# Optimization experiments

Measured on AMD Instinct MI355X. Metric: run time of the kernel, lower is better.

Reference implementation:

```python
import jax, jax.numpy as jnp
import numpy as np

B, H, W, C = 64, 56, 56, 192
HEADS = 6
WIN = (7, 7)
SHIFT = (3, 3)
N = WIN[0] * WIN[1]  # tokens per window = 49
EPS = 1e-5


def _rel_pos_index(ws):
    # standard Swin relative position index, shape (N, N), values in [0, (2wh-1)(2ww-1))
    coords = np.stack(np.meshgrid(np.arange(ws[0]), np.arange(ws[1]), indexing='ij'))
    cf = coords.reshape(2, -1)
    rel = (cf[:, :, None] - cf[:, None, :]).transpose(1, 2, 0)  # N,N,2
    rel[..., 0] += ws[0] - 1
    rel[..., 1] += ws[1] - 1
    rel[..., 0] *= 2 * ws[1] - 1
    return rel.sum(-1)


def _swin_attn_mask(h, w, ws, ss):
    # cyclic-shift attention mask, shape (nW, N, N), values {0, -100}
    img = np.zeros((h, w), dtype=np.float32)
    cnt = 0
    for hs in (slice(0, -ws[0]), slice(-ws[0], -ss[0]), slice(-ss[0], None)):
        for wsl in (slice(0, -ws[1]), slice(-ws[1], -ss[1]), slice(-ss[1], None)):
            img[hs, wsl] = cnt
            cnt += 1
    m = img.reshape(h // ws[0], ws[0], w // ws[1], ws[1]).transpose(0, 2, 1, 3).reshape(-1, N)
    am = m[:, None, :] - m[:, :, None]
    return np.where(am != 0, -100.0, 0.0).astype(np.float32)


def setup_inputs() -> dict:
    key = jax.random.key(0)
    ks = jax.random.split(key, 5)
    x = jax.random.normal(ks[0], (B, H, W, C), dtype=jnp.float32)
    mask_matrix = jnp.asarray(_swin_attn_mask(H, W, WIN, SHIFT))
    gamma = jnp.ones((C,), jnp.float32)
    beta = jnp.zeros((C,), jnp.float32)
    w_qkv = jax.random.normal(ks[1], (C, 3 * C), jnp.float32) * 0.02
    b_qkv = jnp.zeros((3 * C,), jnp.float32)
    rel_table = jax.random.normal(ks[2], ((2 * WIN[0] - 1) * (2 * WIN[1] - 1), HEADS), jnp.float32) * 0.02
    w_proj = jax.random.normal(ks[3], (C, C), jnp.float32) * 0.02
    b_proj = jnp.zeros((C,), jnp.float32)
    return {"x": x, "gamma": gamma, "beta": beta, "w_qkv": w_qkv, "b_qkv": b_qkv,
            "rel_table": rel_table, "w_proj": w_proj, "b_proj": b_proj,
            "mask_matrix": mask_matrix}


def reference(x, gamma, beta, w_qkv, b_qkv, rel_table, w_proj, b_proj, mask_matrix):
    b, h, w, c = x.shape
    hd = c // HEADS
    scale = hd ** -0.5

    # norm1 (LayerNorm over channels)
    mu = jnp.mean(x, axis=-1, keepdims=True)
    var = jnp.var(x, axis=-1, keepdims=True)
    x = (x - mu) * jax.lax.rsqrt(var + EPS) * gamma + beta

    # cyclic shift (H,W divisible by window -> no padding)
    sx = jnp.roll(x, shift=(-SHIFT[0], -SHIFT[1]), axis=(1, 2))

    # window partition -> (B*nW, N, C)
    nh, nw = h // WIN[0], w // WIN[1]
    win = sx.reshape(b, nh, WIN[0], nw, WIN[1], c).transpose(0, 1, 3, 2, 4, 5)
    win = win.reshape(-1, N, c)

    # window attention with relative position bias + shift mask
    qkv = (win @ w_qkv + b_qkv).reshape(-1, N, 3, HEADS, hd).transpose(2, 0, 3, 1, 4)
    q, k, v = qkv[0], qkv[1], qkv[2]  # (B_, heads, N, hd)
    attn = jnp.einsum('bhnd,bhmd->bhnm', q * scale, k)
    rpi = _rel_pos_index(WIN)
    bias = rel_table[rpi.reshape(-1)].reshape(N, N, HEADS).transpose(2, 0, 1)  # heads,N,N
    attn = attn + bias[None]
    nW = mask_matrix.shape[0]
    attn = attn.reshape(b, nW, HEADS, N, N) + mask_matrix[None, :, None]
    attn = jax.nn.softmax(attn.reshape(-1, HEADS, N, N), axis=-1)
    out = jnp.einsum('bhnm,bhmd->bhnd', attn, v).transpose(0, 2, 1, 3).reshape(-1, N, c)
    out = out @ w_proj + b_proj

    # window reverse -> (B,H,W,C)
    out = out.reshape(b, nh, nw, WIN[0], WIN[1], c).transpose(0, 1, 3, 2, 4, 5).reshape(b, h, w, c)

    # reverse cyclic shift
    return jnp.roll(out, shift=(SHIFT[0], SHIFT[1]), axis=(1, 2))
```

## Files before the change

kernel.cpp:

```cpp
#include <hip/hip_runtime.h>
#include <hip/hip_bf16.h>
#include <math.h>

typedef __bf16 bf16;
typedef __bf16 bf16x4 __attribute__((ext_vector_type(4)));
typedef __bf16 bf16x8 __attribute__((ext_vector_type(8)));
typedef float f32x4 __attribute__((ext_vector_type(4)));
typedef unsigned int u32x4 __attribute__((ext_vector_type(4)));

#define NHEADS 6
#define CDIM 192
#define IMG 56
#define NTOK 49
#define SHIFTV 3
#define XSTR 200
#define VSTR 72
#define LOG2E 1.4426950408889634f
#define SCALE 0.17677669529663687f
#define MSKNEG (-100.0f * LOG2E)

#define MFMA(a, b, c) __builtin_amdgcn_mfma_f32_16x16x32_bf16(a, b, c, 0, 0, 0)

static __device__ __forceinline__ unsigned pack2bf(float lo, float hi) {
    unsigned short a = __builtin_bit_cast(unsigned short, (bf16)lo);
    unsigned short b = __builtin_bit_cast(unsigned short, (bf16)hi);
    return (unsigned)a | ((unsigned)b << 16);
}

__global__ void prep_weights(const float* __restrict__ w_qkv, const float* __restrict__ w_proj,
                             bf16* __restrict__ wqkvT, bf16* __restrict__ wprojT) {
    int i = blockIdx.x * 256 + threadIdx.x;
    if (i < 576 * 192) {
        int n = i / 192, k = i % 192;
        wqkvT[i] = (bf16)w_qkv[k * 576 + n];
    }
    if (i < 192 * 192) {
        int n = i / 192, k = i % 192;
        wprojT[i] = (bf16)w_proj[k * 192 + n];
    }
}

__global__ __launch_bounds__(512, 4) void swin_block(
    const float* __restrict__ x, const float* __restrict__ gamma, const float* __restrict__ beta,
    const bf16* __restrict__ wqkvT, const float* __restrict__ b_qkv,
    const float* __restrict__ rel_table, const bf16* __restrict__ wprojT,
    const float* __restrict__ b_proj, float* __restrict__ out)
{
    __shared__ __align__(16) bf16 BufA[64 * XSTR];
    __shared__ __align__(16) bf16 BufB[64 * XSTR];
    __shared__ __align__(16) bf16 VTs[CDIM * VSTR];
    __shared__ bf16 biasS[169 * NHEADS];

    const int blk  = blockIdx.x;
    const int bimg = blk >> 6;
    const int wy   = (blk >> 3) & 7;
    const int wx   = blk & 7;
    const int tid  = threadIdx.x;
    const int wave = tid >> 6;
    const int lane = tid & 63;
    const int lr   = lane & 15;
    const int lq   = lane >> 4;
    const int h0   = wave & 1;
    const int cg   = wave >> 1;

    for (int i = tid; i < 169 * NHEADS; i += 512) biasS[i] = (bf16)(rel_table[i] * LOG2E);

    {
        const int c0 = lr * 12;
        const f32x4 gm0 = *(const f32x4*)&gamma[c0], gm1 = *(const f32x4*)&gamma[c0 + 4], gm2 = *(const f32x4*)&gamma[c0 + 8];
        const f32x4 bt0 = *(const f32x4*)&beta[c0],  bt1 = *(const f32x4*)&beta[c0 + 4],  bt2 = *(const f32x4*)&beta[c0 + 8];
        #pragma unroll
        for (int it = 0; it < 2; ++it) {
            const int t = it * 32 + wave * 4 + lq;
            if (t < NTOK) {
                int ty = t / 7, tx = t % 7;
                int oy = wy * 7 + ty + SHIFTV; if (oy >= IMG) oy -= IMG;
                int ox = wx * 7 + tx + SHIFTV; if (ox >= IMG) ox -= IMG;
                const float* xp = x + (((size_t)bimg * IMG + oy) * IMG + ox) * CDIM + c0;
                f32x4 v0 = *(const f32x4*)(xp), v1 = *(const f32x4*)(xp + 4), v2 = *(const f32x4*)(xp + 8);
                float s = 0.f, ss = 0.f;
                #pragma unroll
                for (int r = 0; r < 4; ++r) {
                    s  += v0[r] + v1[r] + v2[r];
                    ss += v0[r] * v0[r] + v1[r] * v1[r] + v2[r] * v2[r];
                }
                #pragma unroll
                for (int off = 1; off < 16; off <<= 1) { s += __shfl_xor(s, off); ss += __shfl_xor(ss, off); }
                float mu  = s * (1.f / 192.f);
                float var = ss * (1.f / 192.f) - mu * mu;
                float rs  = rsqrtf(var + 1e-5f);
                bf16x4 o0, o1, o2;
                #pragma unroll
                for (int r = 0; r < 4; ++r) {
                    o0[r] = (bf16)((v0[r] - mu) * rs * gm0[r] + bt0[r]);
                    o1[r] = (bf16)((v1[r] - mu) * rs * gm1[r] + bt1[r]);
                    o2[r] = (bf16)((v2[r] - mu) * rs * gm2[r] + bt2[r]);
                }
                *(bf16x4*)&BufA[t * XSTR + c0    ] = o0;
                *(bf16x4*)&BufA[t * XSTR + c0 + 4] = o1;
                *(bf16x4*)&BufA[t * XSTR + c0 + 8] = o2;
            } else {
                bf16x4 z = {(bf16)0.f, (bf16)0.f, (bf16)0.f, (bf16)0.f};
                *(bf16x4*)&BufA[t * XSTR + c0    ] = z;
                *(bf16x4*)&BufA[t * XSTR + c0 + 4] = z;
                *(bf16x4*)&BufA[t * XSTR + c0 + 8] = z;
            }
        }
    }
    __syncthreads();

    {
        bf16x8 afrag[2][6];
        #pragma unroll
        for (int mm = 0; mm < 2; ++mm)
            #pragma unroll
            for (int k = 0; k < 6; ++k)
                afrag[mm][k] = *(const bf16x8*)&BufA[(32 * h0 + 16 * mm + lr) * XSTR + k * 32 + lq * 8];
        __syncthreads();

        const bf16* wbase = wqkvT + (size_t)lr * CDIM + lq * 8;
#define WPTR(nt) (wbase + (size_t)(nt) * (16 * CDIM))
#define LOADW6(dst, p) do { const bf16* _p = (p); \
    _Pragma("unroll") for (int k = 0; k < 6; ++k) dst[k] = *(const bf16x8*)(_p + k * 32); } while (0)
#define COMP_QK(buf, nt, dstb) do { \
    f32x4 a0 = {0.f,0.f,0.f,0.f}, a1 = {0.f,0.f,0.f,0.f}; \
    _Pragma("unroll") for (int k = 0; k < 6; ++k) { \
        a0 = MFMA(buf[k], afrag[0][k], a0); \
        a1 = MFMA(buf[k], afrag[1][k], a1); } \
    const int ccl_ = ((nt) % 12) * 16 + 4 * lq; \
    const f32x4 bq_ = *(const f32x4*)&b_qkv[(nt) * 16 + 4 * lq]; \
    bf16x4 v0_, v1_; \
    _Pragma("unroll") for (int r = 0; r < 4; ++r) { v0_[r] = (bf16)(a0[r] + bq_[r]); v1_[r] = (bf16)(a1[r] + bq_[r]); } \
    *(bf16x4*)&dstb[(32 * h0 + lr) * XSTR + ccl_] = v0_; \
    *(bf16x4*)&dstb[(32 * h0 + 16 + lr) * XSTR + ccl_] = v1_; } while (0)
#define COMP_V(buf, nt) do { \
    f32x4 a0 = {0.f,0.f,0.f,0.f}, a1 = {0.f,0.f,0.f,0.f}; \
    _Pragma("unroll") for (int k = 0; k < 6; ++k) { \
        a0 = MFMA(afrag[0][k], buf[k], a0); \
        a1 = MFMA(afrag[1][k], buf[k], a1); } \
    const int cc_ = ((nt) - 24) * 16 + lr; \
    const float bb_ = b_qkv[384 + cc_]; \
    bf16x4 v0_, v1_; \
    _Pragma("unroll") for (int r = 0; r < 4; ++r) { v0_[r] = (bf16)(a0[r] + bb_); v1_[r] = (bf16)(a1[r] + bb_); } \
    *(bf16x4*)&VTs[cc_ * VSTR + 32 * h0 + 4 * lq] = v0_; \
    *(bf16x4*)&VTs[cc_ * VSTR + 32 * h0 + 16 + 4 * lq] = v1_; } while (0)

        bf16x8 bA[6], bB[6];
        LOADW6(bA, WPTR(cg));
        LOADW6(bB, WPTR(cg + 4));  COMP_QK(bA, cg,      BufB);
        LOADW6(bA, WPTR(cg + 8));  COMP_QK(bB, cg + 4,  BufB);
        LOADW6(bB, WPTR(cg + 12)); COMP_QK(bA, cg + 8,  BufB);
        LOADW6(bA, WPTR(cg + 16)); COMP_QK(bB, cg + 12, BufA);
        LOADW6(bB, WPTR(cg + 20)); COMP_QK(bA, cg + 16, BufA);
        LOADW6(bA, WPTR(cg + 24)); COMP_QK(bB, cg + 20, BufA);
        LOADW6(bB, WPTR(cg + 28)); COMP_V (bA, cg + 24);
        LOADW6(bA, WPTR(cg + 32)); COMP_V (bB, cg + 28);
                                   COMP_V (bA, cg + 32);
    }
    __syncthreads();

    {
        const int m  = wave & 3;
        const int hg = wave >> 2;
        const int i  = 16 * m + lr;
        const int ic = i < NTOK ? i : NTOK - 1;
        const int iy = ic / 7, ix = ic % 7;
        const int ay = wy * 7 + iy, ax = wx * 7 + ix;
        const int ryi = (ay < 49) ? 0 : ((ay < 53) ? 1 : 2);
        const int rxi = (ax < 49) ? 0 : ((ax < 53) ? 1 : 2);
        int   rp[4][4];
        float msk[4][4];
        #pragma unroll
        for (int n = 0; n < 4; ++n)
            #pragma unroll
            for (int r = 0; r < 4; ++r) {
                int j = 16 * n + 4 * lq + r;
                if (j < NTOK) {
                    int jy = j / 7, jx = j % 7;
                    rp[n][r] = ((iy - jy + 6) * 13 + (ix - jx + 6)) * NHEADS;
                    int by = wy * 7 + jy, bx = wx * 7 + jx;
                    int ryj = (by < 49) ? 0 : ((by < 53) ? 1 : 2);
                    int rxj = (bx < 49) ? 0 : ((bx < 53) ? 1 : 2);
                    msk[n][r] = (ryi == ryj && rxi == rxj) ? 0.f : MSKNEG;
                } else { rp[n][r] = 0; msk[n][r] = -1e30f; }
            }
        const int src0 = lr + 32 * (lq & 1);
        const float SC = SCALE * LOG2E;

        #pragma unroll
        for (int hh = 0; hh < 3; ++hh) {
            const int h = hg * 3 + hh;
            bf16x8 bq = *(const bf16x8*)&BufB[(16 * m + lr) * XSTR + h * 32 + lq * 8];
            f32x4 st[4];
            #pragma unroll
            for (int n = 0; n < 4; ++n) {
                bf16x8 ak = *(const bf16x8*)&BufA[(16 * n + lr) * XSTR + h * 32 + lq * 8];
                st[n] = MFMA(ak, bq, (f32x4{0.f, 0.f, 0.f, 0.f}));
            }
            float umax = -1e30f;
            #pragma unroll
            for (int n = 0; n < 4; ++n)
                #pragma unroll
                for (int r = 0; r < 4; ++r) {
                    st[n][r] = fmaf(st[n][r], SC, msk[n][r]) + (float)biasS[rp[n][r] + h];
                    umax = fmaxf(umax, st[n][r]);
                }
            umax = fmaxf(umax, __shfl_xor(umax, 16));
            umax = fmaxf(umax, __shfl_xor(umax, 32));
            float sum = 0.f;
            #pragma unroll
            for (int n = 0; n < 4; ++n)
                #pragma unroll
                for (int r = 0; r < 4; ++r) {
                    float e = exp2f(st[n][r] - umax);
                    st[n][r] = e; sum += e;
                }
            sum += __shfl_xor(sum, 16);
            sum += __shfl_xor(sum, 32);
            const float inv = 1.f / sum;
            unsigned pk[4][2];
            #pragma unroll
            for (int n = 0; n < 4; ++n)
                #pragma unroll
                for (int s = 0; s < 2; ++s)
                    pk[n][s] = pack2bf(st[n][2 * s] * inv, st[n][2 * s + 1] * inv);
            u32x4 ptw0, ptw1;
            #pragma unroll
            for (int w = 0; w < 4; ++w) {
                int srcl = src0 + 16 * (w >> 1);
                int s = w & 1;
                unsigned a0 = (unsigned)__shfl((int)pk[0][s], srcl);
                unsigned b0 = (unsigned)__shfl((int)pk[1][s], srcl);
                unsigned a1 = (unsigned)__shfl((int)pk[2][s], srcl);
                unsigned b1 = (unsigned)__shfl((int)pk[3][s], srcl);
                ptw0[w] = (lq & 2) ? b0 : a0;
                ptw1[w] = (lq & 2) ? b1 : a1;
            }
            bf16x8 bp0 = __builtin_bit_cast(bf16x8, ptw0);
            bf16x8 bp1 = __builtin_bit_cast(bf16x8, ptw1);
            f32x4 ot[2];
            #pragma unroll
            for (int dt = 0; dt < 2; ++dt) {
                const bf16* vrow = &VTs[(h * 32 + 16 * dt + lr) * VSTR + lq * 8];
                bf16x8 av0 = *(const bf16x8*)(vrow);
                bf16x8 av1 = *(const bf16x8*)(vrow + 32);
                ot[dt] = MFMA(av0, bp0, (f32x4{0.f, 0.f, 0.f, 0.f}));
                ot[dt] = MFMA(av1, bp1, ot[dt]);
            }
            #pragma unroll
            for (int dt = 0; dt < 2; ++dt) {
                bf16x4 o4;
                #pragma unroll
                for (int r = 0; r < 4; ++r) o4[r] = (bf16)ot[dt][r];
                *(bf16x4*)&BufB[(16 * m + lr) * XSTR + h * 32 + 16 * dt + 4 * lq] = o4;
            }
        }
    }
    __syncthreads();

    {
        bf16x8 ofrag[2][6];
        #pragma unroll
        for (int mm = 0; mm < 2; ++mm)
            #pragma unroll
            for (int k = 0; k < 6; ++k)
                ofrag[mm][k] = *(const bf16x8*)&BufB[(32 * h0 + 16 * mm + lr) * XSTR + k * 32 + lq * 8];
        float* orow[2];
        bool   valid[2];
        #pragma unroll
        for (int mm = 0; mm < 2; ++mm) {
            const int row = 32 * h0 + 16 * mm + lr;
            valid[mm] = row < NTOK;
            int rr = valid[mm] ? row : 0;
            int ty = rr / 7, tx = rr % 7;
            int oy = wy * 7 + ty + SHIFTV; if (oy >= IMG) oy -= IMG;
            int ox = wx * 7 + tx + SHIFTV; if (ox >= IMG) ox -= IMG;
            orow[mm] = out + (((size_t)bimg * IMG + oy) * IMG + ox) * CDIM;
        }

        const bf16* pbase = wprojT + (size_t)lr * CDIM + lq * 8;
#define PPTR(nt) (pbase + (size_t)(nt) * (16 * CDIM))
#define COMP3(buf, nt) do { \
    f32x4 a0 = {0.f,0.f,0.f,0.f}, a1 = {0.f,0.f,0.f,0.f}; \
    _Pragma("unroll") for (int k = 0; k < 6; ++k) { \
        a0 = MFMA(buf[k], ofrag[0][k], a0); \
        a1 = MFMA(buf[k], ofrag[1][k], a1); } \
    const int c0_ = (nt) * 16 + 4 * lq; \
    const f32x4 bp_ = *(const f32x4*)&b_proj[c0_]; \
    if (valid[0]) { f32x4 v_; _Pragma("unroll") for (int r = 0; r < 4; ++r) v_[r] = a0[r] + bp_[r]; *(f32x4*)&orow[0][c0_] = v_; } \
    if (valid[1]) { f32x4 v_; _Pragma("unroll") for (int r = 0; r < 4; ++r) v_[r] = a1[r] + bp_[r]; *(f32x4*)&orow[1][c0_] = v_; } \
} while (0)

        bf16x8 pA[6], pB[6];
        LOADW6(pA, PPTR(cg));
        LOADW6(pB, PPTR(cg + 4)); COMP3(pA, cg);
        LOADW6(pA, PPTR(cg + 8)); COMP3(pB, cg + 4);
                                  COMP3(pA, cg + 8);
    }
}

extern "C" void kernel_launch(void* const* d_in, const int* in_sizes, int n_in,
                              void* d_out, int out_size, void* d_ws, size_t ws_size,
                              hipStream_t stream) {
    const float* x           = (const float*)d_in[0];
    const float* gamma       = (const float*)d_in[1];
    const float* beta        = (const float*)d_in[2];
    const float* w_qkv       = (const float*)d_in[3];
    const float* b_qkv       = (const float*)d_in[4];
    const float* rel_table   = (const float*)d_in[5];
    const float* w_proj      = (const float*)d_in[6];
    const float* b_proj      = (const float*)d_in[7];
    float* out = (float*)d_out;

    bf16* wqkvT  = (bf16*)d_ws;
    bf16* wprojT = (bf16*)((char*)d_ws + (size_t)576 * 192 * 2);

    prep_weights<<<432, 256, 0, stream>>>(w_qkv, w_proj, wqkvT, wprojT);
    swin_block<<<4096, 512, 0, stream>>>(x, gamma, beta, wqkvT, b_qkv, rel_table,
                                         wprojT, b_proj, out);
}
```

Baseline: 341.4 us.

## Precompute combined bias+mask tables per window class in prep kernel

Builds a global bf16 table holding relative-position bias plus shift mask, pre-scaled by log2e, for four window classes (interior, last row, last column, corner) and all heads, laid out to match the MFMA output fragment. The attention kernel now issues vectorized loads from this table instead of staging rel_table in shared memory and computing index and mask per element. It also runs all three heads' QK MFMAs before any softmax, giving more independent work to overlap. The trade-off is extra register pressure and global/L2 traffic for the table, and the mask is now encoded through the window class rather than computed from absolute coordinates.

```diff
diff --git a/kernel.cpp b/kernel.cpp
--- a/kernel.cpp
+++ b/kernel.cpp
@@ -17,7 +17,6 @@
 #define VSTR 72
 #define LOG2E 1.4426950408889634f
 #define SCALE 0.17677669529663687f
-#define MSKNEG (-100.0f * LOG2E)
 
 #define MFMA(a, b, c) __builtin_amdgcn_mfma_f32_16x16x32_bf16(a, b, c, 0, 0, 0)
 
@@ -28,7 +27,9 @@
 }
 
 __global__ void prep_weights(const float* __restrict__ w_qkv, const float* __restrict__ w_proj,
-                             bf16* __restrict__ wqkvT, bf16* __restrict__ wprojT) {
+                             const float* __restrict__ rel_table,
+                             bf16* __restrict__ wqkvT, bf16* __restrict__ wprojT,
+                             bf16* __restrict__ biasG) {
     int i = blockIdx.x * 256 + threadIdx.x;
     if (i < 576 * 192) {
         int n = i / 192, k = i % 192;
@@ -38,18 +39,30 @@
         int n = i / 192, k = i % 192;
         wprojT[i] = (bf16)w_proj[k * 192 + n];
     }
+    if (i < 24 * 64 * 64) {
+        int j = i & 63, ii = (i >> 6) & 63, t = i >> 12;
+        int h = t % 6, c = t / 6;
+        float val = -100.f;
+        if (ii < 49 && j < 49) {
+            int iy = ii / 7, ix = ii % 7, jy = j / 7, jx = j % 7;
+            int rp = (iy - jy + 6) * 13 + (ix - jx + 6);
+            bool ym = !(c & 2) || ((iy < 4) == (jy < 4));
+            bool xm = !(c & 1) || ((ix < 4) == (jx < 4));
+            val = rel_table[rp * 6 + h] + ((ym && xm) ? 0.f : -100.f);
+        }
+        biasG[i] = (bf16)(val * LOG2E);
+    }
 }
 
 __global__ __launch_bounds__(512, 4) void swin_block(
     const float* __restrict__ x, const float* __restrict__ gamma, const float* __restrict__ beta,
     const bf16* __restrict__ wqkvT, const float* __restrict__ b_qkv,
-    const float* __restrict__ rel_table, const bf16* __restrict__ wprojT,
+    const bf16* __restrict__ biasG, const bf16* __restrict__ wprojT,
     const float* __restrict__ b_proj, float* __restrict__ out)
 {
     __shared__ __align__(16) bf16 BufA[64 * XSTR];
     __shared__ __align__(16) bf16 BufB[64 * XSTR];
     __shared__ __align__(16) bf16 VTs[CDIM * VSTR];
-    __shared__ bf16 biasS[169 * NHEADS];
 
     const int blk  = blockIdx.x;
     const int bimg = blk >> 6;
@@ -62,8 +75,6 @@
     const int lq   = lane >> 4;
     const int h0   = wave & 1;
     const int cg   = wave >> 1;
-
-    for (int i = tid; i < 169 * NHEADS; i += 512) biasS[i] = (bf16)(rel_table[i] * LOG2E);
 
     {
         const int c0 = lr * 12;
@@ -162,48 +173,40 @@
     {
         const int m  = wave & 3;
         const int hg = wave >> 2;
-        const int i  = 16 * m + lr;
-        const int ic = i < NTOK ? i : NTOK - 1;
-        const int iy = ic / 7, ix = ic % 7;
-        const int ay = wy * 7 + iy, ax = wx * 7 + ix;
-        const int ryi = (ay < 49) ? 0 : ((ay < 53) ? 1 : 2);
-        const int rxi = (ax < 49) ? 0 : ((ax < 53) ? 1 : 2);
-        int   rp[4][4];
-        float msk[4][4];
-        #pragma unroll
-        for (int n = 0; n < 4; ++n)
-            #pragma unroll
-            for (int r = 0; r < 4; ++r) {
-                int j = 16 * n + 4 * lq + r;
-                if (j < NTOK) {
-                    int jy = j / 7, jx = j % 7;
-                    rp[n][r] = ((iy - jy + 6) * 13 + (ix - jx + 6)) * NHEADS;
-                    int by = wy * 7 + jy, bx = wx * 7 + jx;
-                    int ryj = (by < 49) ? 0 : ((by < 53) ? 1 : 2);
-                    int rxj = (bx < 49) ? 0 : ((bx < 53) ? 1 : 2);
-                    msk[n][r] = (ryi == ryj && rxi == rxj) ? 0.f : MSKNEG;
-                } else { rp[n][r] = 0; msk[n][r] = -1e30f; }
-            }
+        const int cls = ((wy == 7) ? 2 : 0) | ((wx == 7) ? 1 : 0);
+        const bf16* bgp = biasG + (((size_t)cls * 6 + hg * 3) * 64 + (16 * m + lr)) * 64 + 4 * lq;
         const int src0 = lr + 32 * (lq & 1);
         const float SC = SCALE * LOG2E;
 
+        bf16x4 b4[3][4];
+        #pragma unroll
+        for (int hh = 0; hh < 3; ++hh)
+            #pragma unroll
+            for (int n = 0; n < 4; ++n)
+                b4[hh][n] = *(const bf16x4*)(bgp + hh * 4096 + 16 * n);
+
+        f32x4 st[3][4];
         #pragma unroll
         for (int hh = 0; hh < 3; ++hh) {
             const int h = hg * 3 + hh;
             bf16x8 bq = *(const bf16x8*)&BufB[(16 * m + lr) * XSTR + h * 32 + lq * 8];
-            f32x4 st[4];
             #pragma unroll
             for (int n = 0; n < 4; ++n) {
                 bf16x8 ak = *(const bf16x8*)&BufA[(16 * n + lr) * XSTR + h * 32 + lq * 8];
-                st[n] = MFMA(ak, bq, (f32x4{0.f, 0.f, 0.f, 0.f}));
-            }
+                st[hh][n] = MFMA(ak, bq, (f32x4{0.f, 0.f, 0.f, 0.f}));
+            }
+        }
+
+        #pragma unroll
+        for (int hh = 0; hh < 3; ++hh) {
+            const int h = hg * 3 + hh;
             float umax = -1e30f;
             #pragma unroll
             for (int n = 0; n < 4; ++n)
                 #pragma unroll
                 for (int r = 0; r < 4; ++r) {
-                    st[n][r] = fmaf(st[n][r], SC, msk[n][r]) + (float)biasS[rp[n][r] + h];
-                    umax = fmaxf(umax, st[n][r]);
+                    st[hh][n][r] = fmaf(st[hh][n][r], SC, (float)b4[hh][n][r]);
+                    umax = fmaxf(umax, st[hh][n][r]);
                 }
             umax = fmaxf(umax, __shfl_xor(umax, 16));
             umax = fmaxf(umax, __shfl_xor(umax, 32));
@@ -212,8 +215,8 @@
             for (int n = 0; n < 4; ++n)
                 #pragma unroll
                 for (int r = 0; r < 4; ++r) {
-                    float e = exp2f(st[n][r] - umax);
-                    st[n][r] = e; sum += e;
+                    float e = exp2f(st[hh][n][r] - umax);
+                    st[hh][n][r] = e; sum += e;
                 }
             sum += __shfl_xor(sum, 16);
             sum += __shfl_xor(sum, 32);
@@ -223,7 +226,7 @@
             for (int n = 0; n < 4; ++n)
                 #pragma unroll
                 for (int s = 0; s < 2; ++s)
-                    pk[n][s] = pack2bf(st[n][2 * s] * inv, st[n][2 * s + 1] * inv);
+                    pk[n][s] = pack2bf(st[hh][n][2 * s] * inv, st[hh][n][2 * s + 1] * inv);
             u32x4 ptw0, ptw1;
             #pragma unroll
             for (int w = 0; w < 4; ++w) {
@@ -313,9 +316,10 @@
     float* out = (float*)d_out;
 
     bf16* wqkvT  = (bf16*)d_ws;
-    bf16* wprojT = (bf16*)((char*)d_ws + (size_t)576 * 192 * 2);
-
-    prep_weights<<<432, 256, 0, stream>>>(w_qkv, w_proj, wqkvT, wprojT);
-    swin_block<<<4096, 512, 0, stream>>>(x, gamma, beta, wqkvT, b_qkv, rel_table,
+    bf16* wprojT = (bf16*)((char*)d_ws + 221184);
+    bf16* biasG  = (bf16*)((char*)d_ws + 221184 + 73728);
+
+    prep_weights<<<432, 256, 0, stream>>>(w_qkv, w_proj, rel_table, wqkvT, wprojT, biasG);
+    swin_block<<<4096, 512, 0, stream>>>(x, gamma, beta, wqkvT, b_qkv, biasG,
                                          wprojT, b_proj, out);
 }
```

Result: slower. 378.8 us (+11.0%).
